# Kernel optimization log

Measured on AMD Instinct MI355X. Metric: run time of the kernel, lower is better.

Reference implementation:

```python
import jax, jax.numpy as jnp
import numpy as np
from math import sqrt

SIZE = 4096
NR_CORES = 2
RANK = 16
D = 64  # core_size: D**NR_CORES == SIZE


def setup_inputs() -> dict:
    key = jax.random.key(0)
    k_x, k_c0, k_c1, k_b = jax.random.split(key, 4)
    t = 1.0 / sqrt(SIZE)
    sigma = (t * sqrt(RANK) ** (1 - NR_CORES)) ** (1.0 / NR_CORES)
    x = jax.random.normal(k_x, (2, 4096, SIZE), dtype=jnp.float32)
    core0 = sigma * jax.random.normal(k_c0, (D, D, D, RANK, 1), dtype=jnp.float32)
    core1 = sigma * jax.random.normal(k_c1, (D, D, D, 1, RANK), dtype=jnp.float32)
    bias = sqrt(1.0 / SIZE) * jax.random.uniform(k_b, (SIZE,), minval=-1.0, maxval=1.0, dtype=jnp.float32)
    return {"x": x, "core0": core0, "core1": core1, "bias": bias}


def _btt_forward(x, cores, bias):
    d, c, size = D, NR_CORES, SIZE
    G = cores[0]  # (d,...,d, r, 1)
    for idx, core in enumerate(cores[1:]):
        j = d ** (idx + 1)
        i = d ** (c - idx - 1)
        core_r = core.reshape(j, d, i, core.shape[-2], core.shape[-1])
        G_r = G.reshape(j, d ** (idx + 1), i, G.shape[-2], G.shape[-1])
        # contract rank dim b: (j,x,i,cb) x (j,y,i,ba) -> (j,x,y,i,c,a)
        G = jnp.einsum('jxicb,jyiba->jxyica', core_r, G_r)
    G = G.reshape(size, size)
    out = x.reshape(-1, size) @ G + bias
    return out.reshape(x.shape)


def reference(x, core0, core1, bias):
    return _btt_forward(x, [core0, core1], bias)
```

## Files before the change

kernel.cpp:

```cpp
#include <hip/hip_runtime.h>
#include <hip/hip_bf16.h>
#include <stdint.h>
#include <stddef.h>

using bf16 = __hip_bfloat16;

typedef __attribute__((ext_vector_type(4))) float f32x4;
typedef __attribute__((ext_vector_type(8))) short bf16x8;
typedef __attribute__((ext_vector_type(4))) unsigned short u16x4;

#define K_DIM 4096
#define M_ROWS 8192
#define BM 256
#define BN 128
#define BK 32
#define NTT (K_DIM / BK)
#define MT2 (M_ROWS / BM)
#define NT2 (K_DIM / BN)

__global__ void conv_bf16(const float* __restrict__ in, bf16* __restrict__ outb, int n4) {
  int idx = blockIdx.x * blockDim.x + threadIdx.x;
  int stride = gridDim.x * blockDim.x;
  for (int k = idx; k < n4; k += stride) {
    f32x4 v = ((const f32x4*)in)[k];
    bf16 tmp[4];
    tmp[0] = __float2bfloat16(v.x);
    tmp[1] = __float2bfloat16(v.y);
    tmp[2] = __float2bfloat16(v.z);
    tmp[3] = __float2bfloat16(v.w);
    ((u16x4*)outb)[k] = *(const u16x4*)tmp;
  }
}

__global__ void build_gt(const float* __restrict__ core0, const float* __restrict__ core1,
                         bf16* __restrict__ GT) {
  int j = blockIdx.x >> 6;
  int i = blockIdx.x & 63;
  __shared__ float c0s[64][16];
  __shared__ float c1s[64][16];
  int t = threadIdx.x;
#pragma unroll
  for (int rep = 0; rep < 4; ++rep) {
    int idx = rep * 256 + t;
    int row = idx >> 4;
    int b = idx & 15;
    size_t base = ((size_t)(j * 64 + row) * 64 + i) * 16 + b;
    c1s[row][b] = core1[base];
    c0s[row][b] = core0[base];
  }
  __syncthreads();
  int x = t & 63;
  int ys = t >> 6;
  float r1[16];
#pragma unroll
  for (int b = 0; b < 16; ++b) r1[b] = c1s[x][b];
#pragma unroll
  for (int yy = 0; yy < 16; ++yy) {
    int y = ys * 16 + yy;
    float acc = 0.f;
#pragma unroll
    for (int b = 0; b < 16; ++b) acc += r1[b] * c0s[y][b];
    GT[((size_t)(y * 64 + i) << 12) + (size_t)(j * 64 + x)] = __float2bfloat16(acc);
  }
}

__device__ __forceinline__ void gload_lds16(const bf16* g, bf16* l) {
  __builtin_amdgcn_global_load_lds(
      (const __attribute__((address_space(1))) unsigned int*)(g),
      (__attribute__((address_space(3))) unsigned int*)(l),
      16, 0, 0);
}

#define BARRIER() __builtin_amdgcn_s_barrier()
#define SP1() __builtin_amdgcn_s_setprio(1)
#define SP0() __builtin_amdgcn_s_setprio(0)
#define VMCNT0() asm volatile("s_waitcnt vmcnt(0)" ::: "memory")

__global__ __launch_bounds__(256, 2)
void gemm_xg(const bf16* __restrict__ Xb, const bf16* __restrict__ GT,
             const float* __restrict__ bias, float* __restrict__ out) {
  __shared__ bf16 As[2][128 * 64];
  __shared__ bf16 Bs[2][64 * 64];

  int bid = blockIdx.x;
  int sb = (bid & 7) * (MT2 * NT2 / 8) + (bid >> 3);
  int bm = sb >> 5;
  int bn = sb & 31;

  int t = threadIdx.x;
  int lane = t & 63;
  int wid = t >> 6;

  int ssr = t >> 3;
  int sslot = t & 7;
  int sp = sslot ^ (ssr & 7);
  int srowpar = sp >> 2;
  int skofs = (sp & 3) * 8;
  const bf16* gA0 = Xb + ((size_t)(bm * BM + 2 * ssr + srowpar) * K_DIM) + skofs;
  const bf16* gB0 = GT + ((size_t)(bn * BN + 2 * ssr + srowpar) * K_DIM) + skofs;
  int ldst = ssr * 64 + sslot * 8;

  auto stage = [&](int buf, int kt) {
#pragma unroll
    for (int h = 0; h < 4; ++h)
      gload_lds16(gA0 + (size_t)(h * 64) * K_DIM + kt * BK,
                  &As[buf][h * 32 * 64 + ldst]);
#pragma unroll
    for (int h = 0; h < 2; ++h)
      gload_lds16(gB0 + (size_t)(h * 64) * K_DIM + kt * BK,
                  &Bs[buf][h * 32 * 64 + ldst]);
  };

  int wm = wid >> 1;
  int wn = wid & 1;
  int lr = lane & 15;
  int g4 = lane >> 4;
  int lh = lr >> 1;
  int lp = lr & 1;
  int aslot = ((lp << 2) | g4) ^ lh;
  int aoff = (wm * 64 + lh) * 64 + aslot * 8;
  int boff = (wn * 32 + lh) * 64 + aslot * 8;

  f32x4 acc[8][4] = {};

  auto compute = [&](const bf16* Ac, const bf16* Bc) {
    bf16x8 af[8], bf4[4];
#pragma unroll
    for (int mi = 0; mi < 8; ++mi)
      af[mi] = *(const bf16x8*)&Ac[aoff + mi * 512];
#pragma unroll
    for (int ni = 0; ni < 4; ++ni)
      bf4[ni] = *(const bf16x8*)&Bc[boff + ni * 512];
    SP1();
#pragma unroll
    for (int mi = 0; mi < 8; ++mi)
#pragma unroll
      for (int ni = 0; ni < 4; ++ni)
        acc[mi][ni] = __builtin_amdgcn_mfma_f32_16x16x32_bf16(
            af[mi], bf4[ni], acc[mi][ni], 0, 0, 0);
    SP0();
  };

  stage(0, 0);
  VMCNT0();
  BARRIER();

#pragma unroll 1
  for (int i = 0; i < NTT / 2; ++i) {
    stage(1, 2 * i + 1);
    compute(&As[0][0], &Bs[0][0]);
    VMCNT0();
    BARRIER();
    if (i + 1 < NTT / 2) stage(0, 2 * i + 2);
    compute(&As[1][0], &Bs[1][0]);
    VMCNT0();
    BARRIER();
  }

  int colbase = bn * BN + wn * 64 + lr;
  int rowbase = bm * BM + wm * 128 + g4 * 4;
#pragma unroll
  for (int ni = 0; ni < 4; ++ni) {
    int col = colbase + ni * 16;
    float bv = bias[col];
#pragma unroll
    for (int mi = 0; mi < 8; ++mi) {
#pragma unroll
      for (int r = 0; r < 4; ++r) {
        int row = rowbase + mi * 16 + r;
        out[(size_t)row * K_DIM + col] = acc[mi][ni][r] + bv;
      }
    }
  }
}

extern "C" void kernel_launch(void* const* d_in, const int* in_sizes, int n_in,
                              void* d_out, int out_size, void* d_ws, size_t ws_size,
                              hipStream_t stream) {
  const float* x     = (const float*)d_in[0];
  const float* core0 = (const float*)d_in[1];
  const float* core1 = (const float*)d_in[2];
  const float* bias  = (const float*)d_in[3];
  float* out = (float*)d_out;

  bf16* Xb = (bf16*)d_ws;
  bf16* GT = (bf16*)((char*)d_ws + (size_t)M_ROWS * K_DIM * sizeof(bf16));

  conv_bf16<<<2048, 256, 0, stream>>>(x, Xb, (M_ROWS * K_DIM) / 4);
  build_gt<<<4096, 256, 0, stream>>>(core0, core1, GT);
  gemm_xg<<<MT2 * NT2, 256, 0, stream>>>(Xb, GT, bias, out);
}
```

Measured before the change: 340.7 us.

## Enlarge GEMM tile to 256x256x64 with 128x128 per-wave subtiles and split fragment loads

Grows the GEMM block tile from 256x128 with K-step 32 to 256x256 with K-step 64. Each wave now computes a 128x128 output tile with an 8x8 accumulator array. LDS fragment reads are split into halves and interleaved with the MFMA quadrants, and the LDS swizzle is redone for the wider K rows. The aim is higher arithmetic intensity per global and LDS byte and fewer barriers per K. In exchange it uses far more registers and 128KB of LDS, dropping occupancy to one block per CU and halving the number of blocks.

```diff
diff --git a/kernel.cpp b/kernel.cpp
--- a/kernel.cpp
+++ b/kernel.cpp
@@ -12,9 +12,9 @@
 #define K_DIM 4096
 #define M_ROWS 8192
 #define BM 256
-#define BN 128
-#define BK 32
-#define NTT (K_DIM / BK)
+#define BN 256
+#define BK 64
+#define NT (K_DIM / BK)
 #define MT2 (M_ROWS / BM)
 #define NT2 (K_DIM / BN)
 
@@ -71,73 +71,89 @@
       16, 0, 0);
 }
 
-#define BARRIER() __builtin_amdgcn_s_barrier()
+#define BARRIER() asm volatile("s_barrier" ::: "memory")
+#define VMCNT0() asm volatile("s_waitcnt vmcnt(0)" ::: "memory")
 #define SP1() __builtin_amdgcn_s_setprio(1)
 #define SP0() __builtin_amdgcn_s_setprio(0)
-#define VMCNT0() asm volatile("s_waitcnt vmcnt(0)" ::: "memory")
-
-__global__ __launch_bounds__(256, 2)
+
+__global__ __launch_bounds__(256, 1)
 void gemm_xg(const bf16* __restrict__ Xb, const bf16* __restrict__ GT,
              const float* __restrict__ bias, float* __restrict__ out) {
-  __shared__ bf16 As[2][128 * 64];
-  __shared__ bf16 Bs[2][64 * 64];
+  __shared__ bf16 As[2][BM * BK];
+  __shared__ bf16 Bs[2][BN * BK];
 
   int bid = blockIdx.x;
   int sb = (bid & 7) * (MT2 * NT2 / 8) + (bid >> 3);
-  int bm = sb >> 5;
-  int bn = sb & 31;
+  int bm = sb >> 4;
+  int bn = sb & 15;
 
   int t = threadIdx.x;
   int lane = t & 63;
   int wid = t >> 6;
 
-  int ssr = t >> 3;
-  int sslot = t & 7;
-  int sp = sslot ^ (ssr & 7);
-  int srowpar = sp >> 2;
-  int skofs = (sp & 3) * 8;
-  const bf16* gA0 = Xb + ((size_t)(bm * BM + 2 * ssr + srowpar) * K_DIM) + skofs;
-  const bf16* gB0 = GT + ((size_t)(bn * BN + 2 * ssr + srowpar) * K_DIM) + skofs;
-  int ldst = ssr * 64 + sslot * 8;
+  int srow = t >> 3;
+  int scol = t & 7;
+  int sxor = scol ^ (srow & 7);
+  const bf16* gA0 = Xb + ((size_t)(bm * BM + srow) * K_DIM) + sxor * 8;
+  const bf16* gB0 = GT + ((size_t)(bn * BN + srow) * K_DIM) + sxor * 8;
+  int lbase = srow * BK + scol * 8;
+
+  bf16* As0 = &As[0][0];
+  bf16* Bs0 = &Bs[0][0];
 
   auto stage = [&](int buf, int kt) {
-#pragma unroll
-    for (int h = 0; h < 4; ++h)
-      gload_lds16(gA0 + (size_t)(h * 64) * K_DIM + kt * BK,
-                  &As[buf][h * 32 * 64 + ldst]);
-#pragma unroll
-    for (int h = 0; h < 2; ++h)
-      gload_lds16(gB0 + (size_t)(h * 64) * K_DIM + kt * BK,
-                  &Bs[buf][h * 32 * 64 + ldst]);
+    bf16* la = As0 + buf * (BM * BK) + lbase;
+    bf16* lb = Bs0 + buf * (BN * BK) + lbase;
+#pragma unroll
+    for (int h = 0; h < 8; ++h)
+      gload_lds16(gA0 + (size_t)(h * 32) * K_DIM + (size_t)kt * BK,
+                  la + h * 32 * BK);
+#pragma unroll
+    for (int h = 0; h < 8; ++h)
+      gload_lds16(gB0 + (size_t)(h * 32) * K_DIM + (size_t)kt * BK,
+                  lb + h * 32 * BK);
   };
 
   int wm = wid >> 1;
   int wn = wid & 1;
   int lr = lane & 15;
   int g4 = lane >> 4;
-  int lh = lr >> 1;
-  int lp = lr & 1;
-  int aslot = ((lp << 2) | g4) ^ lh;
-  int aoff = (wm * 64 + lh) * 64 + aslot * 8;
-  int boff = (wn * 32 + lh) * 64 + aslot * 8;
-
-  f32x4 acc[8][4] = {};
-
-  auto compute = [&](const bf16* Ac, const bf16* Bc) {
-    bf16x8 af[8], bf4[4];
-#pragma unroll
-    for (int mi = 0; mi < 8; ++mi)
-      af[mi] = *(const bf16x8*)&Ac[aoff + mi * 512];
-#pragma unroll
-    for (int ni = 0; ni < 4; ++ni)
-      bf4[ni] = *(const bf16x8*)&Bc[boff + ni * 512];
+  int x7 = lr & 7;
+  int swk0 = ((g4 ^ x7) << 3);
+  int swk1 = (((4 + g4) ^ x7) << 3);
+  int abase = (wm * 128 + lr) * BK;
+  int bbase = (wn * 128 + lr) * BK;
+
+  f32x4 acc[8][8] = {};
+  bf16x8 a0[4][2], a1[4][2];
+  bf16x8 b0[4][2], b1[4][2];
+
+  auto rdA = [&](bf16x8 (&av)[4][2], const bf16* Ap, int half) {
+#pragma unroll
+    for (int mi = 0; mi < 4; ++mi) {
+      int off = abase + (half * 4 + mi) * 1024;
+      av[mi][0] = *(const bf16x8*)&Ap[off + swk0];
+      av[mi][1] = *(const bf16x8*)&Ap[off + swk1];
+    }
+  };
+  auto rdB = [&](bf16x8 (&bv)[4][2], const bf16* Bp, int half) {
+#pragma unroll
+    for (int ni = 0; ni < 4; ++ni) {
+      int off = bbase + (half * 4 + ni) * 1024;
+      bv[ni][0] = *(const bf16x8*)&Bp[off + swk0];
+      bv[ni][1] = *(const bf16x8*)&Bp[off + swk1];
+    }
+  };
+  auto MQ = [&](int mh, int nh, bf16x8 (&av)[4][2], bf16x8 (&bv)[4][2]) {
     SP1();
 #pragma unroll
-    for (int mi = 0; mi < 8; ++mi)
-#pragma unroll
-      for (int ni = 0; ni < 4; ++ni)
-        acc[mi][ni] = __builtin_amdgcn_mfma_f32_16x16x32_bf16(
-            af[mi], bf4[ni], acc[mi][ni], 0, 0, 0);
+    for (int kk = 0; kk < 2; ++kk)
+#pragma unroll
+      for (int mi = 0; mi < 4; ++mi)
+#pragma unroll
+        for (int ni = 0; ni < 4; ++ni)
+          acc[mh * 4 + mi][nh * 4 + ni] = __builtin_amdgcn_mfma_f32_16x16x32_bf16(
+              av[mi][kk], bv[ni][kk], acc[mh * 4 + mi][nh * 4 + ni], 0, 0, 0);
     SP0();
   };
 
@@ -146,21 +162,30 @@
   BARRIER();
 
 #pragma unroll 1
-  for (int i = 0; i < NTT / 2; ++i) {
-    stage(1, 2 * i + 1);
-    compute(&As[0][0], &Bs[0][0]);
+  for (int kt = 0; kt < NT; ++kt) {
+    int cur = kt & 1;
+    const bf16* Ac = As0 + cur * (BM * BK);
+    const bf16* Bc = Bs0 + cur * (BN * BK);
+
+    if (kt + 1 < NT) stage(cur ^ 1, kt + 1);
+
+    rdA(a0, Ac, 0);
+    rdB(b0, Bc, 0);
+    rdA(a1, Ac, 1);
+    MQ(0, 0, a0, b0);
+    rdB(b1, Bc, 1);
+    MQ(1, 0, a1, b0);
+    MQ(0, 1, a0, b1);
+    MQ(1, 1, a1, b1);
+
     VMCNT0();
     BARRIER();
-    if (i + 1 < NTT / 2) stage(0, 2 * i + 2);
-    compute(&As[1][0], &Bs[1][0]);
-    VMCNT0();
-    BARRIER();
-  }
-
-  int colbase = bn * BN + wn * 64 + lr;
+  }
+
+  int colbase = bn * BN + wn * 128 + lr;
   int rowbase = bm * BM + wm * 128 + g4 * 4;
 #pragma unroll
-  for (int ni = 0; ni < 4; ++ni) {
+  for (int ni = 0; ni < 8; ++ni) {
     int col = colbase + ni * 16;
     float bv = bias[col];
 #pragma unroll
```

New measurement: 427.3 us. +25.4%, slower.
